# Kernel tuning notes

Hardware: AMD Instinct MI355X
Metric: run time of the kernel (lower is better)

The kernel has to match this reference:

```python
import jax, jax.numpy as jnp
import numpy as np

COMMITMENT_COST = 0.25
DECAY = 0.99
EPSILON = 1e-05
NUM_EMBEDDINGS = 1024
EMBEDDING_DIM = 256


def setup_inputs() -> dict:
    key = jax.random.key(0)
    k1, k2, k3 = jax.random.split(key, 3)
    inputs = jax.random.normal(k1, (64, 32, 32, EMBEDDING_DIM), dtype=jnp.float32)
    embedding = jax.random.normal(k2, (NUM_EMBEDDINGS, EMBEDDING_DIM), dtype=jnp.float32)
    ema_cluster_size = jnp.zeros((NUM_EMBEDDINGS,), dtype=jnp.float32)
    ema_w = jax.random.normal(k3, (NUM_EMBEDDINGS, EMBEDDING_DIM), dtype=jnp.float32)
    return {"inputs": inputs, "embedding": embedding,
            "ema_cluster_size": ema_cluster_size, "ema_w": ema_w}


def reference(inputs, embedding, ema_cluster_size, ema_w):
    K, D = embedding.shape
    orig_shape = inputs.shape
    flat = inputs.reshape(-1, D)  # [N, D]

    distances = (jnp.sum(flat * flat, axis=-1, keepdims=True)
                 + jnp.sum(embedding * embedding, axis=-1)[None, :]
                 - 2.0 * flat @ embedding.T)
    idx = jnp.argmin(distances, axis=-1)  # [N] int

    # one-hot @ embedding == gather
    quantized = embedding[idx].reshape(orig_shape)

    # EMA state update (training mode)
    counts = jax.ops.segment_sum(jnp.ones_like(idx, dtype=flat.dtype), idx,
                                 num_segments=K)  # encodings.sum(0)
    new_cluster_size = DECAY * ema_cluster_size + (1.0 - DECAY) * counts
    dw = jax.ops.segment_sum(flat, idx, num_segments=K)  # encodings.T @ flat
    new_ema_w = DECAY * ema_w + (1.0 - DECAY) * dw
    n = jnp.sum(new_cluster_size)
    normalized = (new_cluster_size + EPSILON) / (n + K * EPSILON) * n
    new_embedding = new_ema_w / normalized[:, None]

    commitment_loss = COMMITMENT_COST * jnp.mean((quantized - inputs) ** 2)
    codebook_loss = jnp.mean((quantized - inputs) ** 2)

    # straight-through estimator
    quantized_st = inputs + jax.lax.stop_gradient(quantized - inputs)
    codes = idx.reshape(orig_shape[:-1])
    return (quantized_st, codes, commitment_loss, codebook_loss,
            new_embedding, new_cluster_size, new_ema_w)
```

## Files before the change

kernel.cpp:

```cpp
#include <hip/hip_runtime.h>

#define NV 65536
#define KN 1024
#define DD 256
#define DECAY_F 0.99f
#define OMD_F (1.0f - 0.99f)
#define EPS_F 1e-5f

typedef __attribute__((ext_vector_type(8))) short short8;
typedef __attribute__((ext_vector_type(16))) float f32x16;

__device__ __forceinline__ void gl_lds16(const void* g, void* l) {
  __builtin_amdgcn_global_load_lds(
      (const __attribute__((address_space(1))) unsigned int*)g,
      (__attribute__((address_space(3))) unsigned int*)l, 16, 0, 0);
}

__device__ __forceinline__ void bf16_split(float v, short& hi, short& lo) {
  unsigned u = __float_as_uint(v);
  unsigned hr = (u + 0x7FFFu + ((u >> 16) & 1u)) >> 16;
  float hf = __uint_as_float(hr << 16);
  float rem = v - hf;
  unsigned u2 = __float_as_uint(rem);
  unsigned lr = (u2 + 0x7FFFu + ((u2 >> 16) & 1u)) >> 16;
  hi = (short)hr;
  lo = (short)lr;
}

__device__ __forceinline__ void split8(float4 a, float4 b, short8& h,
                                       short8& l) {
  float v[8] = {a.x, a.y, a.z, a.w, b.x, b.y, b.z, b.w};
  #pragma unroll
  for (int j = 0; j < 8; j++) {
    short hh, ll;
    bf16_split(v[j], hh, ll);
    h[j] = hh; l[j] = ll;
  }
}

__global__ __launch_bounds__(256) void prep_small(
    const float* __restrict__ emb, const float* __restrict__ ema_w,
    short* __restrict__ eT, float* __restrict__ eSq,
    float* __restrict__ outW, float* __restrict__ sseSlots) {
  const int b = blockIdx.x;
  if (b < 32) {
    const int cc = b >> 3, dc = b & 7;
    const int c = threadIdx.x;
    const float* src = emb + (cc * 256 + c) * 256 + dc * 32;
    short* tile = eT + b * 16384;
    #pragma unroll
    for (int db = 0; db < 4; db++) {
      float v[8];
      *(float4*)(v + 0) = *(const float4*)(src + db * 8);
      *(float4*)(v + 4) = *(const float4*)(src + db * 8 + 4);
      short8 h, l;
      #pragma unroll
      for (int j = 0; j < 8; j++) {
        short hh, ll;
        bf16_split(v[j], hh, ll);
        h[j] = hh; l[j] = ll;
      }
      *(short8*)(tile + ((0 * 4 + db) * 256 + c) * 8) = h;
      *(short8*)(tile + ((1 * 4 + db) * 256 + c) * 8) = l;
    }
  } else if (b < 288) {
    const int lane = threadIdx.x & 63;
    const int row = (b - 32) * 4 + (threadIdx.x >> 6);
    const float4 v = *(const float4*)(emb + row * DD + lane * 4);
    float s = v.x * v.x + v.y * v.y + v.z * v.z + v.w * v.w;
    #pragma unroll
    for (int off = 32; off > 0; off >>= 1) s += __shfl_down(s, off, 64);
    if (lane == 0) eSq[row] = s;
  } else if (b < 800) {
    const int i = (b - 288) * 512 + threadIdx.x * 2;
    const float2 w = *(const float2*)(ema_w + i);
    float2 o;
    o.x = DECAY_F * w.x;
    o.y = DECAY_F * w.y;
    *(float2*)(outW + i) = o;
  } else {
    if (threadIdx.x < 256) sseSlots[threadIdx.x] = 0.0f;
  }
}

__global__ __launch_bounds__(256, 2) void argmin_mfma(
    const float* __restrict__ x, const float* __restrict__ emb,
    const short* __restrict__ eT, const float* __restrict__ eSq,
    float* __restrict__ outQ, float* __restrict__ outCodes,
    int* __restrict__ idxFinal, float* __restrict__ sseSlots) {
  __shared__ __align__(16) char uS[67584];
  __shared__ float eSqS[1024];
  __shared__ float sseW[4];

  float2* dbAll = (float2*)uS;

  const int tid = threadIdx.x;
  const int lane = tid & 63;
  const int wid = tid >> 6;
  const int l31 = lane & 31;
  const int lh = lane >> 5;
  const int qBase = blockIdx.x * 128 + wid * 32;

  *(float4*)(eSqS + tid * 4) = *(const float4*)(eSq + tid * 4);
  __syncthreads();

  float2* dbW = dbAll + wid * (64 * 33);

  float b1d = 3.4e38f, b2d = 3.4e38f;
  int b1k = 0, b2k = 1;

  const int qRow = (qBase + l31) * DD;

  const int wbase = wid * 1024;
  const int lane16 = lane * 16;

  for (int cc = 0; cc < 4; cc++) {
    __syncthreads();

    {
      const char* src = (const char*)(eT + (cc * 8 + 0) * 16384);
      #pragma unroll
      for (int i = 0; i < 8; i++)
        gl_lds16(src + i * 4096 + wbase + lane16, uS + i * 4096 + wbase);
    }

    f32x16 acc[8];
    #pragma unroll
    for (int ct = 0; ct < 8; ct++)
      #pragma unroll
      for (int i = 0; i < 16; i++) acc[ct][i] = 0.0f;

    float es2[8];
    #pragma unroll
    for (int ct = 0; ct < 8; ct++) es2[ct] = eSqS[cc * 256 + ct * 32 + l31];

    for (int dc = 0; dc < 8; dc++) {
      const int cur = dc & 1;
      const short* eS = (const short*)(uS + cur * 32768);

      float4 ra0, rb0, ra1, rb1;
      {
        const float* xr = x + qRow + dc * 32 + lh * 8;
        ra0 = *(const float4*)(xr);
        rb0 = *(const float4*)(xr + 4);
        ra1 = *(const float4*)(xr + 16);
        rb1 = *(const float4*)(xr + 20);
      }
      __builtin_amdgcn_sched_barrier(0);

      if (dc < 7) {
        const char* src = (const char*)(eT + (cc * 8 + dc + 1) * 16384);
        char* dst = uS + (cur ^ 1) * 32768;
        #pragma unroll
        for (int i = 0; i < 8; i++)
          gl_lds16(src + i * 4096 + wbase + lane16, dst + i * 4096 + wbase);
        asm volatile("s_waitcnt vmcnt(12)" ::: "memory");
      } else {
        asm volatile("s_waitcnt vmcnt(4)" ::: "memory");
      }
      __builtin_amdgcn_s_barrier();
      asm volatile("" ::: "memory");

      short8 ahi0, alo0, ahi1, alo1;
      split8(ra0, rb0, ahi0, alo0);
      split8(ra1, rb1, ahi1, alo1);

      #pragma unroll
      for (int ks = 0; ks < 2; ks++) {
        const short8 ahi = ks ? ahi1 : ahi0;
        const short8 alo = ks ? alo1 : alo0;
        const int db = ks * 2 + lh;
        #pragma unroll
        for (int ct = 0; ct < 8; ct++) {
          const int cL = ct * 32 + l31;
          const short8 bhi = *(const short8*)(eS + ((0 * 4 + db) * 256 + cL) * 8);
          const short8 blo = *(const short8*)(eS + ((1 * 4 + db) * 256 + cL) * 8);
          acc[ct] = __builtin_amdgcn_mfma_f32_32x32x16_bf16(ahi, bhi, acc[ct], 0, 0, 0);
          acc[ct] = __builtin_amdgcn_mfma_f32_32x32x16_bf16(ahi, blo, acc[ct], 0, 0, 0);
          acc[ct] = __builtin_amdgcn_mfma_f32_32x32x16_bf16(alo, bhi, acc[ct], 0, 0, 0);
        }
      }

      asm volatile("" ::: "memory");
      __builtin_amdgcn_s_barrier();
      asm volatile("" ::: "memory");
    }

    __syncthreads();

    #pragma unroll
    for (int r = 0; r < 16; r++) {
      const int row = (r & 3) + 8 * (r >> 2) + 4 * lh;
      float cb1 = 3.4e38f, cb2 = 3.4e38f;
      int ck1 = 0, ck2 = 0;
      #pragma unroll
      for (int ct = 0; ct < 8; ct++) {
        const float dd = es2[ct] - 2.0f * acc[ct][r];
        const int k = cc * 256 + ct * 32 + l31;
        if (dd < cb1) { cb2 = cb1; ck2 = ck1; cb1 = dd; ck1 = k; }
        else if (dd < cb2) { cb2 = dd; ck2 = k; }
      }
      dbW[(l31 * 2 + 0) * 33 + row] = make_float2(cb1, __int_as_float(ck1));
      dbW[(l31 * 2 + 1) * 33 + row] = make_float2(cb2, __int_as_float(ck2));
    }
    __syncthreads();

    #pragma unroll
    for (int i = 0; i < 32; i++) {
      const float2 c = dbW[(lh * 32 + i) * 33 + l31];
      const float dd = c.x;
      const int k = __float_as_int(c.y);
      if (dd < b1d) { b2d = b1d; b2k = b1k; b1d = dd; b1k = k; }
      else if (dd < b2d) { b2d = dd; b2k = k; }
    }
  }

  {
    const float p1d = __shfl_xor(b1d, 32, 64);
    const int p1k = __shfl_xor(b1k, 32, 64);
    const float p2d = __shfl_xor(b2d, 32, 64);
    const int p2k = __shfl_xor(b2k, 32, 64);
    if ((p1d < b1d) || (p1d == b1d && p1k < b1k)) {
      b2d = b1d; b2k = b1k; b1d = p1d; b1k = p1k;
    } else if ((p1d < b2d) || (p1d == b2d && p1k < b2k)) {
      b2d = p1d; b2k = p1k;
    }
    if ((p2d < b1d) || (p2d == b1d && p2k < b1k)) {
      b2d = b1d; b2k = b1k; b1d = p2d; b1k = p2k;
    } else if ((p2d < b2d) || (p2d == b2d && p2k < b2k)) {
      b2d = p2d; b2k = p2k;
    }
  }

  float sseAcc = 0.0f;
  for (int qb = 0; qb < 32; qb += 4) {
    int k1[4], k2[4];
    #pragma unroll
    for (int j = 0; j < 4; j++) {
      k1[j] = __shfl(b1k, qb + j, 64);
      k2[j] = __shfl(b2k, qb + j, 64);
    }
    float4 xv[4], e1[4], e2[4];
    #pragma unroll
    for (int j = 0; j < 4; j++) {
      const int n = qBase + qb + j;
      xv[j] = *(const float4*)(x + n * DD + lane * 4);
      e1[j] = *(const float4*)(emb + k1[j] * DD + lane * 4);
      e2[j] = *(const float4*)(emb + k2[j] * DD + lane * 4);
    }
    #pragma unroll
    for (int j = 0; j < 4; j++) {
      const int n = qBase + qb + j;
      float p1 = e1[j].x * (e1[j].x - 2.0f * xv[j].x) +
                 e1[j].y * (e1[j].y - 2.0f * xv[j].y) +
                 e1[j].z * (e1[j].z - 2.0f * xv[j].z) +
                 e1[j].w * (e1[j].w - 2.0f * xv[j].w);
      float p2 = e2[j].x * (e2[j].x - 2.0f * xv[j].x) +
                 e2[j].y * (e2[j].y - 2.0f * xv[j].y) +
                 e2[j].z * (e2[j].z - 2.0f * xv[j].z) +
                 e2[j].w * (e2[j].w - 2.0f * xv[j].w);
      #pragma unroll
      for (int m = 32; m > 0; m >>= 1) {
        p1 += __shfl_xor(p1, m, 64);
        p2 += __shfl_xor(p2, m, 64);
      }
      const bool pick2 = (p2 < p1) || (p2 == p1 && k2[j] < k1[j]);
      const int ksel = pick2 ? k2[j] : k1[j];
      const float4 ev = pick2 ? e2[j] : e1[j];

      *(float4*)(outQ + n * DD + lane * 4) = ev;

      const float d0 = ev.x - xv[j].x, d1 = ev.y - xv[j].y,
                  d2 = ev.z - xv[j].z, d3 = ev.w - xv[j].w;
      float s = d0 * d0 + d1 * d1 + d2 * d2 + d3 * d3;
      #pragma unroll
      for (int m = 32; m > 0; m >>= 1) s += __shfl_down(s, m, 64);
      if (lane == 0) {
        sseAcc += s;
        idxFinal[n] = ksel;
        outCodes[n] = (float)ksel;
      }
    }
  }
  if (lane == 0) sseW[wid] = sseAcc;
  __syncthreads();
  if (tid == 0) {
    const float t = (sseW[0] + sseW[1]) + (sseW[2] + sseW[3]);
    atomicAdd(&sseSlots[blockIdx.x & 255], t);
  }
}

__global__ __launch_bounds__(1024) void scan_scatter_fin(
    const int* __restrict__ idxFinal, const float* __restrict__ ema_cs,
    const float* __restrict__ sseSlots, int* __restrict__ perm,
    float* __restrict__ norm, float* __restrict__ outCS,
    float* __restrict__ outLoss) {
  __shared__ int hist[1024];
  __shared__ int si[1024];
  __shared__ int cur[1024];
  __shared__ float red[1024];
  const int t = threadIdx.x;

  hist[t] = 0;
  __syncthreads();
  for (int i = t; i < NV; i += 1024) atomicAdd(&hist[idxFinal[i]], 1);
  __syncthreads();
  const int v = hist[t];

  si[t] = v;
  __syncthreads();
  #pragma unroll
  for (int off = 1; off < 1024; off <<= 1) {
    const int add = (t >= off) ? si[t - off] : 0;
    __syncthreads();
    si[t] += add;
    __syncthreads();
  }
  cur[t] = si[t] - v;

  const float ncs = DECAY_F * ema_cs[t] + OMD_F * (float)v;
  outCS[t] = ncs;
  red[t] = ncs;
  __syncthreads();
  #pragma unroll
  for (int s = 512; s > 0; s >>= 1) {
    if (t < s) red[t] += red[t + s];
    __syncthreads();
  }
  const float n = red[0];
  __syncthreads();
  norm[t] = (ncs + EPS_F) / (n + (float)KN * EPS_F) * n;

  red[t] = (t < 256) ? sseSlots[t] : 0.0f;
  __syncthreads();
  #pragma unroll
  for (int s = 512; s > 0; s >>= 1) {
    if (t < s) red[t] += red[t + s];
    __syncthreads();
  }
  if (t == 0) {
    const float mse = red[0] * (1.0f / 16777216.0f);
    outLoss[0] = 0.25f * mse;
    outLoss[1] = mse;
  }
  __syncthreads();

  for (int i = t; i < NV; i += 1024) {
    const int k = idxFinal[i];
    const int pos = atomicAdd(&cur[k], 1);
    perm[pos] = (k << 16) | i;
  }
}

__global__ __launch_bounds__(256) void dw_sum(const float* __restrict__ x,
                                              const int* __restrict__ perm,
                                              float* __restrict__ outW) {
  __shared__ int sp[128];
  const int tid = threadIdx.x;
  if (tid < 128) sp[tid] = perm[blockIdx.x * 128 + tid];
  __syncthreads();
  const int w = tid >> 6;
  const int l = tid & 63;
  const int* wp = sp + w * 32;

  float4 acc = make_float4(0.0f, 0.0f, 0.0f, 0.0f);
  int kcur = wp[0] >> 16;

  #pragma unroll
  for (int c = 0; c < 4; c++) {
    float4 v[8];
    int kk[8];
    #pragma unroll
    for (int j = 0; j < 8; j++) {
      const int p = wp[c * 8 + j];
      kk[j] = p >> 16;
      v[j] = *(const float4*)(x + (long)(p & 0xFFFF) * DD + l * 4);
    }
    #pragma unroll
    for (int j = 0; j < 8; j++) {
      if (kk[j] != kcur) {
        float* drow = outW + kcur * DD + l * 4;
        atomicAdd(drow + 0, OMD_F * acc.x);
        atomicAdd(drow + 1, OMD_F * acc.y);
        atomicAdd(drow + 2, OMD_F * acc.z);
        atomicAdd(drow + 3, OMD_F * acc.w);
        acc = make_float4(0.0f, 0.0f, 0.0f, 0.0f);
        kcur = kk[j];
      }
      acc.x += v[j].x; acc.y += v[j].y;
      acc.z += v[j].z; acc.w += v[j].w;
    }
  }
  {
    float* drow = outW + kcur * DD + l * 4;
    atomicAdd(drow + 0, OMD_F * acc.x);
    atomicAdd(drow + 1, OMD_F * acc.y);
    atomicAdd(drow + 2, OMD_F * acc.z);
    atomicAdd(drow + 3, OMD_F * acc.w);
  }
}

__global__ __launch_bounds__(256) void emb_div(
    const float* __restrict__ outW, const float* __restrict__ norm,
    float* __restrict__ outEmb) {
  const int i = blockIdx.x * 256 + threadIdx.x;
  outEmb[i] = outW[i] / norm[i >> 8];
}

extern "C" void kernel_launch(void* const* d_in, const int* in_sizes, int n_in,
                              void* d_out, int out_size, void* d_ws, size_t ws_size,
                              hipStream_t stream) {
  const float* x = (const float*)d_in[0];
  const float* emb = (const float*)d_in[1];
  const float* ema_cs = (const float*)d_in[2];
  const float* ema_w = (const float*)d_in[3];
  float* out = (float*)d_out;
  float* ws = (float*)d_ws;

  float* eSq = ws + 0;
  float* sseSlots = ws + 1024;
  float* norm = ws + 1280;
  int* idxFinal = (int*)(ws + 2304);
  int* perm = (int*)(ws + 67840);

  float* outQ = out;
  float* outCodes = out + 16777216;
  float* outLoss = out + 16842752;
  float* outEmb = out + 16842754;
  float* outCS = out + 17104898;
  float* outW = out + 17105922;

  short* eT = (short*)(out + 16842756);

  prep_small<<<801, 256, 0, stream>>>(emb, ema_w, eT, eSq, outW, sseSlots);
  argmin_mfma<<<NV / 128, 256, 0, stream>>>(x, emb, eT, eSq, outQ, outCodes,
                                            idxFinal, sseSlots);
  scan_scatter_fin<<<1, 1024, 0, stream>>>(idxFinal, ema_cs, sseSlots, perm,
                                           norm, outCS, outLoss);
  dw_sum<<<NV / 128, 256, 0, stream>>>(x, perm, outW);
  emb_div<<<KN * DD / 256, 256, 0, stream>>>(outW, norm, outEmb);
}
```

Before: 317.7 us.

## Fuse dw segment sum, EMA update and embedding divide into per-code kernel

Replaces the atomic-based dw_sum plus separate emb_div and the ema_w pre-scaling pass with one kernel that launches a block per codebook entry. Each block reads its cluster's segment of the sorted permutation (start and count now exported by the scan kernel), reduces the input rows in registers and shared memory, and writes both new_ema_w and new_embedding directly. This removes the float atomics, one kernel launch and an extra pass over the 1 MB state. The trade-off is load imbalance when clusters have very uneven sizes, since one block must sum a large cluster on its own.

```diff
diff --git a/kernel.cpp b/kernel.cpp
--- a/kernel.cpp
+++ b/kernel.cpp
@@ -39,9 +39,8 @@
 }
 
 __global__ __launch_bounds__(256) void prep_small(
-    const float* __restrict__ emb, const float* __restrict__ ema_w,
-    short* __restrict__ eT, float* __restrict__ eSq,
-    float* __restrict__ outW, float* __restrict__ sseSlots) {
+    const float* __restrict__ emb, short* __restrict__ eT,
+    float* __restrict__ eSq, float* __restrict__ sseSlots) {
   const int b = blockIdx.x;
   if (b < 32) {
     const int cc = b >> 3, dc = b & 7;
@@ -71,13 +70,6 @@
     #pragma unroll
     for (int off = 32; off > 0; off >>= 1) s += __shfl_down(s, off, 64);
     if (lane == 0) eSq[row] = s;
-  } else if (b < 800) {
-    const int i = (b - 288) * 512 + threadIdx.x * 2;
-    const float2 w = *(const float2*)(ema_w + i);
-    float2 o;
-    o.x = DECAY_F * w.x;
-    o.y = DECAY_F * w.y;
-    *(float2*)(outW + i) = o;
   } else {
     if (threadIdx.x < 256) sseSlots[threadIdx.x] = 0.0f;
   }
@@ -293,6 +285,7 @@
 __global__ __launch_bounds__(1024) void scan_scatter_fin(
     const int* __restrict__ idxFinal, const float* __restrict__ ema_cs,
     const float* __restrict__ sseSlots, int* __restrict__ perm,
+    int* __restrict__ starts, int* __restrict__ cnts,
     float* __restrict__ norm, float* __restrict__ outCS,
     float* __restrict__ outLoss) {
   __shared__ int hist[1024];
@@ -316,7 +309,10 @@
     si[t] += add;
     __syncthreads();
   }
-  cur[t] = si[t] - v;
+  const int excl = si[t] - v;
+  cur[t] = excl;
+  starts[t] = excl;
+  cnts[t] = v;
 
   const float ncs = DECAY_F * ema_cs[t] + OMD_F * (float)v;
   outCS[t] = ncs;
@@ -352,59 +348,62 @@
   }
 }
 
-__global__ __launch_bounds__(256) void dw_sum(const float* __restrict__ x,
-                                              const int* __restrict__ perm,
-                                              float* __restrict__ outW) {
-  __shared__ int sp[128];
+__global__ __launch_bounds__(256) void dw_fin(
+    const float* __restrict__ x, const int* __restrict__ perm,
+    const int* __restrict__ starts, const int* __restrict__ cnts,
+    const float* __restrict__ ema_w, const float* __restrict__ norm,
+    float* __restrict__ outEmb, float* __restrict__ outW) {
+  const int k = blockIdx.x;
+  const int start = starts[k];
+  const int cnt = cnts[k];
   const int tid = threadIdx.x;
-  if (tid < 128) sp[tid] = perm[blockIdx.x * 128 + tid];
-  __syncthreads();
   const int w = tid >> 6;
   const int l = tid & 63;
-  const int* wp = sp + w * 32;
+
+  __shared__ float4 red[3][64];
 
   float4 acc = make_float4(0.0f, 0.0f, 0.0f, 0.0f);
-  int kcur = wp[0] >> 16;
-
-  #pragma unroll
-  for (int c = 0; c < 4; c++) {
-    float4 v[8];
-    int kk[8];
-    #pragma unroll
-    for (int j = 0; j < 8; j++) {
-      const int p = wp[c * 8 + j];
-      kk[j] = p >> 16;
-      v[j] = *(const float4*)(x + (long)(p & 0xFFFF) * DD + l * 4);
-    }
-    #pragma unroll
-    for (int j = 0; j < 8; j++) {
-      if (kk[j] != kcur) {
-        float* drow = outW + kcur * DD + l * 4;
-        atomicAdd(drow + 0, OMD_F * acc.x);
-        atomicAdd(drow + 1, OMD_F * acc.y);
-        atomicAdd(drow + 2, OMD_F * acc.z);
-        atomicAdd(drow + 3, OMD_F * acc.w);
-        acc = make_float4(0.0f, 0.0f, 0.0f, 0.0f);
-        kcur = kk[j];
-      }
-      acc.x += v[j].x; acc.y += v[j].y;
-      acc.z += v[j].z; acc.w += v[j].w;
-    }
-  }
-  {
-    float* drow = outW + kcur * DD + l * 4;
-    atomicAdd(drow + 0, OMD_F * acc.x);
-    atomicAdd(drow + 1, OMD_F * acc.y);
-    atomicAdd(drow + 2, OMD_F * acc.z);
-    atomicAdd(drow + 3, OMD_F * acc.w);
-  }
-}
-
-__global__ __launch_bounds__(256) void emb_div(
-    const float* __restrict__ outW, const float* __restrict__ norm,
-    float* __restrict__ outEmb) {
-  const int i = blockIdx.x * 256 + threadIdx.x;
-  outEmb[i] = outW[i] / norm[i >> 8];
+
+  for (int base = w * 16; base < cnt; base += 64) {
+    int nn[16];
+    #pragma unroll
+    for (int j = 0; j < 16; j++)
+      nn[j] = (base + j < cnt) ? (perm[start + base + j] & 0xFFFF) : -1;
+    float4 v[16];
+    #pragma unroll
+    for (int j = 0; j < 16; j++)
+      if (nn[j] >= 0)
+        v[j] = *(const float4*)(x + (long)nn[j] * DD + l * 4);
+    #pragma unroll
+    for (int j = 0; j < 16; j++)
+      if (nn[j] >= 0) {
+        acc.x += v[j].x; acc.y += v[j].y;
+        acc.z += v[j].z; acc.w += v[j].w;
+      }
+  }
+
+  if (w) red[w - 1][l] = acc;
+  __syncthreads();
+  if (w == 0) {
+    float4 s = acc;
+    #pragma unroll
+    for (int j = 0; j < 3; j++) {
+      const float4 r = red[j][l];
+      s.x += r.x; s.y += r.y; s.z += r.z; s.w += r.w;
+    }
+    const float nrm = norm[k];
+    const float4 ew = *(const float4*)(ema_w + k * DD + l * 4);
+    float4 nw;
+    nw.x = DECAY_F * ew.x + OMD_F * s.x;
+    nw.y = DECAY_F * ew.y + OMD_F * s.y;
+    nw.z = DECAY_F * ew.z + OMD_F * s.z;
+    nw.w = DECAY_F * ew.w + OMD_F * s.w;
+    *(float4*)(outW + k * DD + l * 4) = nw;
+    float4 oe;
+    oe.x = nw.x / nrm; oe.y = nw.y / nrm;
+    oe.z = nw.z / nrm; oe.w = nw.w / nrm;
+    *(float4*)(outEmb + k * DD + l * 4) = oe;
+  }
 }
 
 extern "C" void kernel_launch(void* const* d_in, const int* in_sizes, int n_in,
@@ -420,8 +419,10 @@
   float* eSq = ws + 0;
   float* sseSlots = ws + 1024;
   float* norm = ws + 1280;
-  int* idxFinal = (int*)(ws + 2304);
-  int* perm = (int*)(ws + 67840);
+  int* starts = (int*)(ws + 2304);
+  int* cnts = (int*)(ws + 3328);
+  int* idxFinal = (int*)(ws + 4352);
+  int* perm = (int*)(ws + 69888);
 
   float* outQ = out;
   float* outCodes = out + 16777216;
@@ -432,11 +433,12 @@
 
   short* eT = (short*)(out + 16842756);
 
-  prep_small<<<801, 256, 0, stream>>>(emb, ema_w, eT, eSq, outW, sseSlots);
+  prep_small<<<289, 256, 0, stream>>>(emb, eT, eSq, sseSlots);
   argmin_mfma<<<NV / 128, 256, 0, stream>>>(x, emb, eT, eSq, outQ, outCodes,
                                             idxFinal, sseSlots);
   scan_scatter_fin<<<1, 1024, 0, stream>>>(idxFinal, ema_cs, sseSlots, perm,
-                                           norm, outCS, outLoss);
-  dw_sum<<<NV / 128, 256, 0, stream>>>(x, perm, outW);
-  emb_div<<<KN * DD / 256, 256, 0, stream>>>(outW, norm, outEmb);
-}
+                                           starts, cnts, norm, outCS,
+                                           outLoss);
+  dw_fin<<<KN, 256, 0, stream>>>(x, perm, starts, cnts, ema_w, norm, outEmb,
+                                 outW);
+}
```

After: 417.6 us. 31.4% more time.
